# Optimization experiments

Measured on AMD Instinct MI355X. Metric: run time of the kernel, lower is better.

Reference implementation:

```python
import jax, jax.numpy as jnp
import numpy as np

B, I, H = 8192, 1024, 1024

def setup_inputs() -> dict:
    key = jax.random.key(0)
    ks = jax.random.split(key, 6)
    s_in = 1.0 / np.sqrt(I)
    s_h = 1.0 / np.sqrt(H)
    return {
        "x": jax.random.normal(ks[0], (B, I), jnp.float32),
        "h_prev": jax.random.normal(ks[1], (B, H), jnp.float32),
        "c_prev": jax.random.normal(ks[2], (B, H), jnp.float32),
        "Wx": jax.random.normal(ks[3], (4, H, I), jnp.float32) * s_in,   # gate order: input, forget, cell, output
        "Wh": jax.random.normal(ks[4], (4, H, H), jnp.float32) * s_h,
        "bh": jax.random.normal(ks[5], (4, H), jnp.float32) * s_h,
    }

def reference(x, h_prev, c_prev, Wx, Wh, bh):
    # Fused: 2 batched GEMMs for all 4 gates -> [B, 4, H]
    gates = (jnp.einsum('bi,ghi->bgh', x, Wx)
             + jnp.einsum('bk,ghk->bgh', h_prev, Wh)
             + bh[None, :, :])
    i = jax.nn.sigmoid(gates[:, 0])
    f = jax.nn.sigmoid(gates[:, 1])
    g = jnp.tanh(gates[:, 2])
    o = jax.nn.sigmoid(gates[:, 3])
    c_next = f * c_prev + i * g
    h_next = o * jnp.tanh(c_next)
    return (h_next, c_next)
```

## Files before the change

kernel.cpp:

```cpp
#include <hip/hip_runtime.h>
#include <hip/hip_bf16.h>
#include <stdint.h>

#define B_DIM 8192
#define I_DIM 1024
#define H_DIM 1024
#define KTOT  2048
#define NTILES 32

typedef __attribute__((ext_vector_type(8))) short short8;
typedef __attribute__((ext_vector_type(4))) float f32x4;

static __device__ __forceinline__ short f2b(float f) {
    __bf16 h = (__bf16)f;
    return __builtin_bit_cast(short, h);
}

static __device__ __forceinline__ short8 pack8(float4 a, float4 b) {
    short8 s;
    s[0] = f2b(a.x); s[1] = f2b(a.y); s[2] = f2b(a.z); s[3] = f2b(a.w);
    s[4] = f2b(b.x); s[5] = f2b(b.y); s[6] = f2b(b.z); s[7] = f2b(b.w);
    return s;
}

static __device__ __forceinline__ float sigmoid_f(float x) {
    return 1.0f / (1.0f + __expf(-x));
}

static __device__ __forceinline__ float tanh_fast(float x) {
    x = fminf(fmaxf(x, -15.0f), 15.0f);
    float e = __expf(2.0f * x);
    return (e - 1.0f) / (e + 1.0f);
}

static __device__ __forceinline__ void load_lds16(const void* gptr, void* lptr) {
    __builtin_amdgcn_global_load_lds(
        (const __attribute__((address_space(1))) uint32_t*)gptr,
        (__attribute__((address_space(3))) uint32_t*)lptr, 16, 0, 0);
}

#define GA_GROUPS (512 * 32 * 2 * 64)
#define GB_GROUPS (256 * 32 * 2 * 64)

__global__ __launch_bounds__(256) void convert_kernel(
    const float* __restrict__ x, const float* __restrict__ h,
    const float* __restrict__ wx, const float* __restrict__ wh,
    short* __restrict__ Aw, short* __restrict__ Bw)
{
    const int64_t total = (int64_t)GA_GROUPS + GB_GROUPS;
    for (int64_t g = (int64_t)blockIdx.x * blockDim.x + threadIdx.x; g < total;
         g += (int64_t)gridDim.x * blockDim.x) {
        const float* src;
        short* dst;
        if (g < GA_GROUPS) {
            const int lane = (int)(g & 63);
            const int rest = (int)(g >> 6);
            const int kh   = rest & 1;
            const int tk   = (rest >> 1) & 31;
            const int mfrag = rest >> 6;
            const int row = (mfrag << 4) + (lane & 15);
            const int k   = (tk << 6) + (kh << 5) + ((lane >> 4) << 3);
            src = (k < 1024) ? (x + (size_t)row * 1024 + k)
                             : (h + (size_t)row * 1024 + (k - 1024));
            dst = Aw + (size_t)g * 8;
        } else {
            const int64_t gb = g - GA_GROUPS;
            const int lane = (int)(gb & 63);
            const int rest = (int)(gb >> 6);
            const int kh   = rest & 1;
            const int tk   = (rest >> 1) & 31;
            const int nfrag = rest >> 6;
            const int cf   = nfrag & 15;
            const int bn   = nfrag >> 4;
            const int gate = cf & 3;
            const int col  = (bn << 6) + ((cf >> 2) << 4) + (lane & 15);
            const int k    = (tk << 6) + (kh << 5) + ((lane >> 4) << 3);
            src = (k < 1024) ? (wx + ((size_t)(gate << 10) + col) * 1024 + k)
                             : (wh + ((size_t)(gate << 10) + col) * 1024 + (k - 1024));
            dst = Bw + (size_t)gb * 8;
        }
        float4 v0 = ((const float4*)src)[0];
        float4 v1 = ((const float4*)src)[1];
        *(short8*)dst = pack8(v0, v1);
    }
}


#define AOFF(d, kp, f) ((d) * 16384 + (kp) * 8192 + (f) * 512)
#define BOFF(d, kp, f) (32768 + (d) * 16384 + (kp) * 8192 + (f) * 512)

#define STAGE_A(dn, kh, tkp) \
    load_lds16(aSrc0 + (tkp) * 1024 + (kh) * 512, &smem[AOFF(dn, kh, 2 * w)]); \
    load_lds16(aSrc1 + (tkp) * 1024 + (kh) * 512, &smem[AOFF(dn, kh, 2 * w + 1)]);

#define STAGE_B(dn, kh, tkp) \
    load_lds16(bSrc0 + (tkp) * 1024 + (kh) * 512, &smem[BOFF(dn, kh, 2 * w)]); \
    load_lds16(bSrc1 + (tkp) * 1024 + (kh) * 512, &smem[BOFF(dn, kh, 2 * w + 1)]);

#define VM4 asm volatile("s_waitcnt vmcnt(4)" ::: "memory");

#define PH(d, kp, mh, AV, BV, STAGE_STMT, EXTRAWAIT) do { \
    _Pragma("unroll") \
    for (int j = 0; j < 4; ++j) \
        BV[j] = *(const short8*)&smem[BOFF(d, kp, wn * 4 + j) + lane * 8]; \
    _Pragma("unroll") \
    for (int i = 0; i < 4; ++i) \
        AV[i] = *(const short8*)&smem[AOFF(d, kp, wm * 8 + (mh) * 4 + i) + lane * 8]; \
    STAGE_STMT \
    __builtin_amdgcn_s_barrier(); \
    __builtin_amdgcn_s_setprio(1); \
    _Pragma("unroll") \
    for (int i = 0; i < 4; ++i) \
        _Pragma("unroll") \
        for (int j = 0; j < 4; ++j) \
            acc[(mh) * 4 + i][j] = __builtin_amdgcn_mfma_f32_16x16x32_bf16( \
                AV[i], BV[j], acc[(mh) * 4 + i][j], 0, 0, 0); \
    __builtin_amdgcn_s_setprio(0); \
    EXTRAWAIT \
    __builtin_amdgcn_s_barrier(); \
} while (0)

#define TILE(d, tn) do { \
    PH(d, 0, 0, avA, bvA, STAGE_A(d ^ 1, 0, tn), ); \
    PH(d, 0, 1, avB, bvB, STAGE_B(d ^ 1, 0, tn), VM4); \
    PH(d, 1, 0, avA, bvA, STAGE_A(d ^ 1, 1, tn), ); \
    PH(d, 1, 1, avB, bvB, STAGE_B(d ^ 1, 1, tn), VM4); \
} while (0)

__global__ __launch_bounds__(512, 2) void lstm_gemm8_kernel(
    const short* __restrict__ Aw, const short* __restrict__ Bw,
    const float* __restrict__ cprev, const float* __restrict__ bh,
    float* __restrict__ out)
{
    extern __shared__ __align__(16) short smem[];

    int bid = blockIdx.x;
    bid = (bid & 7) * 64 + (bid >> 3);
    const int bm = bid >> 4;
    const int bn = bid & 15;
    const int m0 = bm * 256;
    const int h0 = bn * 64;

    const int t    = threadIdx.x;
    const int lane = t & 63;
    const int w    = t >> 6;
    const int wm   = w >> 2;
    const int wn   = w & 3;
    const int lc   = lane & 15;

    const short* aSrc0 = Aw + (size_t)(bm * 16 + 2 * w + 0) * 32768 + lane * 8;
    const short* aSrc1 = Aw + (size_t)(bm * 16 + 2 * w + 1) * 32768 + lane * 8;
    const short* bSrc0 = Bw + (size_t)(bn * 16 + 2 * w + 0) * 32768 + lane * 8;
    const short* bSrc1 = Bw + (size_t)(bn * 16 + 2 * w + 1) * 32768 + lane * 8;

    f32x4 acc[8][4] = {};
    short8 avA[4], avB[4], bvA[4], bvB[4];

    STAGE_A(0, 0, 0)
    STAGE_B(0, 0, 0)
    STAGE_A(0, 1, 0)
    STAGE_B(0, 1, 0)
    asm volatile("s_waitcnt vmcnt(0)" ::: "memory");
    __builtin_amdgcn_s_barrier();

    #pragma unroll 1
    for (int tk2 = 0; tk2 < 16; ++tk2) {
        const int t1  = 2 * tk2 + 1;
        const int tp1 = (t1 + 1 < NTILES) ? t1 + 1 : t1;
        TILE(0, t1);
        TILE(1, tp1);
    }
    asm volatile("s_waitcnt vmcnt(0)" ::: "memory");

    const int rg = lane >> 4;
    const int h  = h0 + wn * 16 + lc;
    const float b_i = bh[0 * H_DIM + h];
    const float b_f = bh[1 * H_DIM + h];
    const float b_g = bh[2 * H_DIM + h];
    const float b_o = bh[3 * H_DIM + h];

    #pragma unroll
    for (int mf = 0; mf < 8; ++mf) {
        #pragma unroll
        for (int r = 0; r < 4; ++r) {
            const int row = m0 + wm * 128 + mf * 16 + rg * 4 + r;
            const float pi = acc[mf][0][r] + b_i;
            const float pf = acc[mf][1][r] + b_f;
            const float pg = acc[mf][2][r] + b_g;
            const float po = acc[mf][3][r] + b_o;
            const float iv = sigmoid_f(pi);
            const float fv = sigmoid_f(pf);
            const float gv = tanh_fast(pg);
            const float ov = sigmoid_f(po);
            const float cp = cprev[(size_t)row * H_DIM + h];
            const float cn = fv * cp + iv * gv;
            const float hn = ov * tanh_fast(cn);
            out[(size_t)row * H_DIM + h] = hn;
            out[(size_t)B_DIM * H_DIM + (size_t)row * H_DIM + h] = cn;
        }
    }
}

static __device__ __forceinline__ int swz(int row, int k) {
    int byte = (row << 7) + (k << 1);
    byte ^= (row & 7) << 4;
    return byte >> 1;
}

__global__ __launch_bounds__(256, 2) void lstm_fallback_kernel(
    const float* __restrict__ x, const float* __restrict__ hprev,
    const float* __restrict__ cprev, const float* __restrict__ Wx,
    const float* __restrict__ Wh, const float* __restrict__ bh,
    float* __restrict__ out)
{
    __shared__ __align__(16) short As[128 * 64];
    __shared__ __align__(16) short Bs[128 * 64];

    int bid = blockIdx.x;
    bid = (bid & 7) * 256 + (bid >> 3);
    const int mt = bid >> 5;
    const int ht = bid & 31;
    const int m0 = mt * 128;
    const int h0 = ht * 32;

    const int t    = threadIdx.x;
    const int lane = t & 63;
    const int w    = t >> 6;
    const int wr   = w >> 1;
    const int wc   = w & 1;

    const int srow = t >> 3;
    const int sk   = (t & 7) * 8;

    f32x4 acc[4][4] = {};

    #pragma unroll 1
    for (int phase = 0; phase < 2; ++phase) {
        const float* __restrict__ Ap = phase ? hprev : x;
        const float* __restrict__ Bp = phase ? Wh : Wx;
        #pragma unroll 1
        for (int kk = 0; kk < 1024; kk += 64) {
            __syncthreads();
            #pragma unroll
            for (int p = 0; p < 4; ++p) {
                const int row = srow + p * 32;
                const float4* src = (const float4*)(Ap + (size_t)(m0 + row) * I_DIM + kk + sk);
                *(short8*)&As[swz(row, sk)] = pack8(src[0], src[1]);
            }
            #pragma unroll
            for (int p = 0; p < 4; ++p) {
                const int n    = srow + p * 32;
                const int gate = (n >> 4) & 3;
                const int hcol = h0 + ((n >> 6) << 4) + (n & 15);
                const float4* src = (const float4*)(Bp + (size_t)((gate << 10) + hcol) * 1024 + kk + sk);
                *(short8*)&Bs[swz(n, sk)] = pack8(src[0], src[1]);
            }
            __syncthreads();
            #pragma unroll
            for (int ks = 0; ks < 2; ++ks) {
                const int kb = ks * 32 + ((lane >> 4) << 3);
                short8 a[4], b[4];
                #pragma unroll
                for (int m = 0; m < 4; ++m)
                    a[m] = *(const short8*)&As[swz(wr * 64 + m * 16 + (lane & 15), kb)];
                #pragma unroll
                for (int j = 0; j < 4; ++j)
                    b[j] = *(const short8*)&Bs[swz(wc * 64 + j * 16 + (lane & 15), kb)];
                #pragma unroll
                for (int m = 0; m < 4; ++m)
                    #pragma unroll
                    for (int j = 0; j < 4; ++j)
                        acc[m][j] = __builtin_amdgcn_mfma_f32_16x16x32_bf16(a[m], b[j], acc[m][j], 0, 0, 0);
            }
        }
    }

    const int cl = lane & 15;
    const int rg = lane >> 4;
    const int h  = h0 + wc * 16 + cl;
    const float b_i = bh[0 * H_DIM + h];
    const float b_f = bh[1 * H_DIM + h];
    const float b_g = bh[2 * H_DIM + h];
    const float b_o = bh[3 * H_DIM + h];

    #pragma unroll
    for (int m = 0; m < 4; ++m) {
        #pragma unroll
        for (int r = 0; r < 4; ++r) {
            const int row = m0 + wr * 64 + m * 16 + rg * 4 + r;
            const float pi = acc[m][0][r] + b_i;
            const float pf = acc[m][1][r] + b_f;
            const float pg = acc[m][2][r] + b_g;
            const float po = acc[m][3][r] + b_o;
            const float iv = sigmoid_f(pi);
            const float fv = sigmoid_f(pf);
            const float gv = tanh_fast(pg);
            const float ov = sigmoid_f(po);
            const float cp = cprev[(size_t)row * H_DIM + h];
            const float cn = fv * cp + iv * gv;
            const float hn = ov * tanh_fast(cn);
            out[(size_t)row * H_DIM + h] = hn;
            out[(size_t)B_DIM * H_DIM + (size_t)row * H_DIM + h] = cn;
        }
    }
}

extern "C" void kernel_launch(void* const* d_in, const int* in_sizes, int n_in,
                              void* d_out, int out_size, void* d_ws, size_t ws_size,
                              hipStream_t stream) {
    const float* x     = (const float*)d_in[0];
    const float* hprev = (const float*)d_in[1];
    const float* cprev = (const float*)d_in[2];
    const float* Wx    = (const float*)d_in[3];
    const float* Wh    = (const float*)d_in[4];
    const float* bh    = (const float*)d_in[5];
    float* out = (float*)d_out;

    const size_t need = ((size_t)B_DIM * 2048 + (size_t)4096 * 2048) * sizeof(short);
    if (ws_size >= need && d_ws != nullptr) {
        (void)hipFuncSetAttribute((const void*)lstm_gemm8_kernel,
                                  hipFuncAttributeMaxDynamicSharedMemorySize, 131072);
        short* Aw = (short*)d_ws;
        short* Bw = Aw + (size_t)512 * 32768;
        hipLaunchKernelGGL(convert_kernel, dim3(4096), dim3(256), 0, stream,
                           x, hprev, Wx, Wh, Aw, Bw);
        hipLaunchKernelGGL(lstm_gemm8_kernel, dim3(512), dim3(512), 131072, stream,
                           Aw, Bw, cprev, bh, out);
    } else {
        hipLaunchKernelGGL(lstm_fallback_kernel, dim3(2048), dim3(256), 0, stream,
                           x, hprev, cprev, Wx, Wh, bh, out);
    }
}
```

Baseline: 154.2 us.

## Replace 256x64 ping-pong GEMM with smaller 128x64 tile for higher occupancy

The hand-scheduled 256-row tile kernel with 128KB dynamic LDS and multi-phase ping-pong staging is replaced by a 128-row tile kernel using 48KB static LDS, half the accumulators, and a simple double-buffered loop over 64 K-steps of 32. Launch bounds move to 4 blocks per CU and the grid doubles to 1024 blocks, with a new XCD-aware block mapping. The aim is to hide latency through thread-level parallelism instead of intra-wave scheduling. In exchange, each K-step ends with a full vmcnt(0) wait and barrier, and B-tile reuse per block is lower, so global and L2 traffic rises.

```diff
diff --git a/kernel.cpp b/kernel.cpp
--- a/kernel.cpp
+++ b/kernel.cpp
@@ -5,8 +5,6 @@
 #define B_DIM 8192
 #define I_DIM 1024
 #define H_DIM 1024
-#define KTOT  2048
-#define NTILES 32
 
 typedef __attribute__((ext_vector_type(8))) short short8;
 typedef __attribute__((ext_vector_type(4))) float f32x4;
@@ -85,61 +83,20 @@
     }
 }
 
-
-#define AOFF(d, kp, f) ((d) * 16384 + (kp) * 8192 + (f) * 512)
-#define BOFF(d, kp, f) (32768 + (d) * 16384 + (kp) * 8192 + (f) * 512)
-
-#define STAGE_A(dn, kh, tkp) \
-    load_lds16(aSrc0 + (tkp) * 1024 + (kh) * 512, &smem[AOFF(dn, kh, 2 * w)]); \
-    load_lds16(aSrc1 + (tkp) * 1024 + (kh) * 512, &smem[AOFF(dn, kh, 2 * w + 1)]);
-
-#define STAGE_B(dn, kh, tkp) \
-    load_lds16(bSrc0 + (tkp) * 1024 + (kh) * 512, &smem[BOFF(dn, kh, 2 * w)]); \
-    load_lds16(bSrc1 + (tkp) * 1024 + (kh) * 512, &smem[BOFF(dn, kh, 2 * w + 1)]);
-
-#define VM4 asm volatile("s_waitcnt vmcnt(4)" ::: "memory");
-
-#define PH(d, kp, mh, AV, BV, STAGE_STMT, EXTRAWAIT) do { \
-    _Pragma("unroll") \
-    for (int j = 0; j < 4; ++j) \
-        BV[j] = *(const short8*)&smem[BOFF(d, kp, wn * 4 + j) + lane * 8]; \
-    _Pragma("unroll") \
-    for (int i = 0; i < 4; ++i) \
-        AV[i] = *(const short8*)&smem[AOFF(d, kp, wm * 8 + (mh) * 4 + i) + lane * 8]; \
-    STAGE_STMT \
-    __builtin_amdgcn_s_barrier(); \
-    __builtin_amdgcn_s_setprio(1); \
-    _Pragma("unroll") \
-    for (int i = 0; i < 4; ++i) \
-        _Pragma("unroll") \
-        for (int j = 0; j < 4; ++j) \
-            acc[(mh) * 4 + i][j] = __builtin_amdgcn_mfma_f32_16x16x32_bf16( \
-                AV[i], BV[j], acc[(mh) * 4 + i][j], 0, 0, 0); \
-    __builtin_amdgcn_s_setprio(0); \
-    EXTRAWAIT \
-    __builtin_amdgcn_s_barrier(); \
-} while (0)
-
-#define TILE(d, tn) do { \
-    PH(d, 0, 0, avA, bvA, STAGE_A(d ^ 1, 0, tn), ); \
-    PH(d, 0, 1, avB, bvB, STAGE_B(d ^ 1, 0, tn), VM4); \
-    PH(d, 1, 0, avA, bvA, STAGE_A(d ^ 1, 1, tn), ); \
-    PH(d, 1, 1, avB, bvB, STAGE_B(d ^ 1, 1, tn), VM4); \
-} while (0)
-
-__global__ __launch_bounds__(512, 2) void lstm_gemm8_kernel(
+__global__ __launch_bounds__(512, 4) void lstm_gemm_tlp_kernel(
     const short* __restrict__ Aw, const short* __restrict__ Bw,
     const float* __restrict__ cprev, const float* __restrict__ bh,
     float* __restrict__ out)
 {
-    extern __shared__ __align__(16) short smem[];
-
-    int bid = blockIdx.x;
-    bid = (bid & 7) * 64 + (bid >> 3);
-    const int bm = bid >> 4;
-    const int bn = bid & 15;
-    const int m0 = bm * 256;
-    const int h0 = bn * 64;
+    __shared__ __align__(16) short smem[24576];
+
+    const int bid = blockIdx.x;
+    const int xcd = bid & 7;
+    const int c   = bid >> 3;
+    const int bm  = c >> 1;
+    const int bn  = 2 * xcd + (c & 1);
+    const int m0  = bm * 128;
+    const int h0  = bn * 64;
 
     const int t    = threadIdx.x;
     const int lane = t & 63;
@@ -148,29 +105,48 @@
     const int wn   = w & 3;
     const int lc   = lane & 15;
 
-    const short* aSrc0 = Aw + (size_t)(bm * 16 + 2 * w + 0) * 32768 + lane * 8;
-    const short* aSrc1 = Aw + (size_t)(bm * 16 + 2 * w + 1) * 32768 + lane * 8;
-    const short* bSrc0 = Bw + (size_t)(bn * 16 + 2 * w + 0) * 32768 + lane * 8;
+    const short* aSrc  = Aw + (size_t)(bm * 8  + w)         * 32768 + lane * 8;
+    const short* bSrc0 = Bw + (size_t)(bn * 16 + 2 * w)     * 32768 + lane * 8;
     const short* bSrc1 = Bw + (size_t)(bn * 16 + 2 * w + 1) * 32768 + lane * 8;
 
-    f32x4 acc[8][4] = {};
-    short8 avA[4], avB[4], bvA[4], bvB[4];
-
-    STAGE_A(0, 0, 0)
-    STAGE_B(0, 0, 0)
-    STAGE_A(0, 1, 0)
-    STAGE_B(0, 1, 0)
+    f32x4 acc[4][4] = {};
+
+    load_lds16(aSrc,  &smem[w * 512]);
+    load_lds16(bSrc0, &smem[4096 + (2 * w) * 512]);
+    load_lds16(bSrc1, &smem[4096 + (2 * w + 1) * 512]);
     asm volatile("s_waitcnt vmcnt(0)" ::: "memory");
     __builtin_amdgcn_s_barrier();
 
     #pragma unroll 1
-    for (int tk2 = 0; tk2 < 16; ++tk2) {
-        const int t1  = 2 * tk2 + 1;
-        const int tp1 = (t1 + 1 < NTILES) ? t1 + 1 : t1;
-        TILE(0, t1);
-        TILE(1, tp1);
-    }
-    asm volatile("s_waitcnt vmcnt(0)" ::: "memory");
+    for (int tk = 0; tk < 64; ++tk) {
+        const int d  = (tk & 1) * 12288;
+        const int dn = 12288 - d;
+        const int tp = (tk + 1 < 64) ? tk + 1 : tk;
+
+        short8 bv[4], av[4];
+        #pragma unroll
+        for (int j = 0; j < 4; ++j)
+            bv[j] = *(const short8*)&smem[d + 4096 + (wn * 4 + j) * 512 + lane * 8];
+        #pragma unroll
+        for (int i = 0; i < 4; ++i)
+            av[i] = *(const short8*)&smem[d + (wm * 4 + i) * 512 + lane * 8];
+
+        load_lds16(aSrc  + tp * 512, &smem[dn + w * 512]);
+        load_lds16(bSrc0 + tp * 512, &smem[dn + 4096 + (2 * w) * 512]);
+        load_lds16(bSrc1 + tp * 512, &smem[dn + 4096 + (2 * w + 1) * 512]);
+
+        __builtin_amdgcn_s_setprio(1);
+        #pragma unroll
+        for (int i = 0; i < 4; ++i)
+            #pragma unroll
+            for (int j = 0; j < 4; ++j)
+                acc[i][j] = __builtin_amdgcn_mfma_f32_16x16x32_bf16(
+                    av[i], bv[j], acc[i][j], 0, 0, 0);
+        __builtin_amdgcn_s_setprio(0);
+
+        asm volatile("s_waitcnt vmcnt(0)" ::: "memory");
+        __builtin_amdgcn_s_barrier();
+    }
 
     const int rg = lane >> 4;
     const int h  = h0 + wn * 16 + lc;
@@ -180,10 +156,10 @@
     const float b_o = bh[3 * H_DIM + h];
 
     #pragma unroll
-    for (int mf = 0; mf < 8; ++mf) {
+    for (int mf = 0; mf < 4; ++mf) {
         #pragma unroll
         for (int r = 0; r < 4; ++r) {
-            const int row = m0 + wm * 128 + mf * 16 + rg * 4 + r;
+            const int row = m0 + wm * 64 + mf * 16 + rg * 4 + r;
             const float pi = acc[mf][0][r] + b_i;
             const float pf = acc[mf][1][r] + b_f;
             const float pg = acc[mf][2][r] + b_g;
@@ -318,13 +294,11 @@
 
     const size_t need = ((size_t)B_DIM * 2048 + (size_t)4096 * 2048) * sizeof(short);
     if (ws_size >= need && d_ws != nullptr) {
-        (void)hipFuncSetAttribute((const void*)lstm_gemm8_kernel,
-                                  hipFuncAttributeMaxDynamicSharedMemorySize, 131072);
         short* Aw = (short*)d_ws;
         short* Bw = Aw + (size_t)512 * 32768;
         hipLaunchKernelGGL(convert_kernel, dim3(4096), dim3(256), 0, stream,
                            x, hprev, Wx, Wh, Aw, Bw);
-        hipLaunchKernelGGL(lstm_gemm8_kernel, dim3(512), dim3(512), 131072, stream,
+        hipLaunchKernelGGL(lstm_gemm_tlp_kernel, dim3(1024), dim3(512), 0, stream,
                            Aw, Bw, cprev, bh, out);
     } else {
         hipLaunchKernelGGL(lstm_fallback_kernel, dim3(2048), dim3(256), 0, stream,
```

Measured after the change: 149.1 us. 3.4% less time.

## Replace double-buffered K tiles with a four-slot ring prefetching three steps ahead

Applied to the files above, without the earlier changes.

The GEMM main loop moves from a two-buffer scheme (64-wide K tiles split into halves) to a four-slot ring of 32-wide K steps in LDS. Loads are issued three steps ahead, with a vmcnt(8) wait. Each step reuses the B fragments across both M halves, so B is read from LDS once per step instead of once per M half. The aim is deeper latency hiding for global-to-LDS loads. In exchange there are more barriers per K element, since there are twice as many steps, each with three barriers.

```diff
diff --git a/kernel.cpp b/kernel.cpp
--- a/kernel.cpp
+++ b/kernel.cpp
@@ -5,8 +5,6 @@
 #define B_DIM 8192
 #define I_DIM 1024
 #define H_DIM 1024
-#define KTOT  2048
-#define NTILES 32
 
 typedef __attribute__((ext_vector_type(8))) short short8;
 typedef __attribute__((ext_vector_type(4))) float f32x4;
@@ -85,49 +83,10 @@
     }
 }
 
-
-#define AOFF(d, kp, f) ((d) * 16384 + (kp) * 8192 + (f) * 512)
-#define BOFF(d, kp, f) (32768 + (d) * 16384 + (kp) * 8192 + (f) * 512)
-
-#define STAGE_A(dn, kh, tkp) \
-    load_lds16(aSrc0 + (tkp) * 1024 + (kh) * 512, &smem[AOFF(dn, kh, 2 * w)]); \
-    load_lds16(aSrc1 + (tkp) * 1024 + (kh) * 512, &smem[AOFF(dn, kh, 2 * w + 1)]);
-
-#define STAGE_B(dn, kh, tkp) \
-    load_lds16(bSrc0 + (tkp) * 1024 + (kh) * 512, &smem[BOFF(dn, kh, 2 * w)]); \
-    load_lds16(bSrc1 + (tkp) * 1024 + (kh) * 512, &smem[BOFF(dn, kh, 2 * w + 1)]);
-
-#define VM4 asm volatile("s_waitcnt vmcnt(4)" ::: "memory");
-
-#define PH(d, kp, mh, AV, BV, STAGE_STMT, EXTRAWAIT) do { \
-    _Pragma("unroll") \
-    for (int j = 0; j < 4; ++j) \
-        BV[j] = *(const short8*)&smem[BOFF(d, kp, wn * 4 + j) + lane * 8]; \
-    _Pragma("unroll") \
-    for (int i = 0; i < 4; ++i) \
-        AV[i] = *(const short8*)&smem[AOFF(d, kp, wm * 8 + (mh) * 4 + i) + lane * 8]; \
-    STAGE_STMT \
-    __builtin_amdgcn_s_barrier(); \
-    __builtin_amdgcn_s_setprio(1); \
-    _Pragma("unroll") \
-    for (int i = 0; i < 4; ++i) \
-        _Pragma("unroll") \
-        for (int j = 0; j < 4; ++j) \
-            acc[(mh) * 4 + i][j] = __builtin_amdgcn_mfma_f32_16x16x32_bf16( \
-                AV[i], BV[j], acc[(mh) * 4 + i][j], 0, 0, 0); \
-    __builtin_amdgcn_s_setprio(0); \
-    EXTRAWAIT \
-    __builtin_amdgcn_s_barrier(); \
-} while (0)
-
-#define TILE(d, tn) do { \
-    PH(d, 0, 0, avA, bvA, STAGE_A(d ^ 1, 0, tn), ); \
-    PH(d, 0, 1, avB, bvB, STAGE_B(d ^ 1, 0, tn), VM4); \
-    PH(d, 1, 0, avA, bvA, STAGE_A(d ^ 1, 1, tn), ); \
-    PH(d, 1, 1, avB, bvB, STAGE_B(d ^ 1, 1, tn), VM4); \
-} while (0)
-
-__global__ __launch_bounds__(512, 2) void lstm_gemm8_kernel(
+#define AOFF(r, f) ((r) * 16384 + (f) * 512)
+#define BOFF(r, f) ((r) * 16384 + 8192 + (f) * 512)
+
+__global__ __launch_bounds__(512, 2) void lstm_gemm_p8_kernel(
     const short* __restrict__ Aw, const short* __restrict__ Bw,
     const float* __restrict__ cprev, const float* __restrict__ bh,
     float* __restrict__ out)
@@ -148,28 +107,78 @@
     const int wn   = w & 3;
     const int lc   = lane & 15;
 
-    const short* aSrc0 = Aw + (size_t)(bm * 16 + 2 * w + 0) * 32768 + lane * 8;
+    const short* aSrc0 = Aw + (size_t)(bm * 16 + 2 * w)     * 32768 + lane * 8;
     const short* aSrc1 = Aw + (size_t)(bm * 16 + 2 * w + 1) * 32768 + lane * 8;
-    const short* bSrc0 = Bw + (size_t)(bn * 16 + 2 * w + 0) * 32768 + lane * 8;
+    const short* bSrc0 = Bw + (size_t)(bn * 16 + 2 * w)     * 32768 + lane * 8;
     const short* bSrc1 = Bw + (size_t)(bn * 16 + 2 * w + 1) * 32768 + lane * 8;
 
     f32x4 acc[8][4] = {};
-    short8 avA[4], avB[4], bvA[4], bvB[4];
-
-    STAGE_A(0, 0, 0)
-    STAGE_B(0, 0, 0)
-    STAGE_A(0, 1, 0)
-    STAGE_B(0, 1, 0)
-    asm volatile("s_waitcnt vmcnt(0)" ::: "memory");
+
+#define SA(r, p) \
+    load_lds16(aSrc0 + (p) * 512, &smem[AOFF(r, 2 * w)]); \
+    load_lds16(aSrc1 + (p) * 512, &smem[AOFF(r, 2 * w + 1)]);
+#define SB(r, p) \
+    load_lds16(bSrc0 + (p) * 512, &smem[BOFF(r, 2 * w)]); \
+    load_lds16(bSrc1 + (p) * 512, &smem[BOFF(r, 2 * w + 1)]);
+
+#define STEP(r, pr, p) do { \
+    short8 bv[4], av[4]; \
+    _Pragma("unroll") \
+    for (int j = 0; j < 4; ++j) \
+        bv[j] = *(const short8*)&smem[BOFF(r, wn * 4 + j) + lane * 8]; \
+    _Pragma("unroll") \
+    for (int i = 0; i < 4; ++i) \
+        av[i] = *(const short8*)&smem[AOFF(r, wm * 8 + i) + lane * 8]; \
+    SA(pr, p) \
+    __builtin_amdgcn_s_barrier(); \
+    __builtin_amdgcn_s_setprio(1); \
+    _Pragma("unroll") \
+    for (int i = 0; i < 4; ++i) \
+        _Pragma("unroll") \
+        for (int j = 0; j < 4; ++j) \
+            acc[i][j] = __builtin_amdgcn_mfma_f32_16x16x32_bf16( \
+                av[i], bv[j], acc[i][j], 0, 0, 0); \
+    __builtin_amdgcn_s_setprio(0); \
+    __builtin_amdgcn_s_barrier(); \
+    short8 aw[4]; \
+    _Pragma("unroll") \
+    for (int i = 0; i < 4; ++i) \
+        aw[i] = *(const short8*)&smem[AOFF(r, wm * 8 + 4 + i) + lane * 8]; \
+    SB(pr, p) \
+    __builtin_amdgcn_s_barrier(); \
+    __builtin_amdgcn_s_setprio(1); \
+    _Pragma("unroll") \
+    for (int i = 0; i < 4; ++i) \
+        _Pragma("unroll") \
+        for (int j = 0; j < 4; ++j) \
+            acc[4 + i][j] = __builtin_amdgcn_mfma_f32_16x16x32_bf16( \
+                aw[i], bv[j], acc[4 + i][j], 0, 0, 0); \
+    __builtin_amdgcn_s_setprio(0); \
+    asm volatile("s_waitcnt vmcnt(8)" ::: "memory"); \
+    __builtin_amdgcn_s_barrier(); \
+} while (0)
+
+    SA(0, 0) SB(0, 0)
+    SA(1, 1) SB(1, 1)
+    SA(2, 2) SB(2, 2)
+    asm volatile("s_waitcnt vmcnt(8)" ::: "memory");
     __builtin_amdgcn_s_barrier();
 
     #pragma unroll 1
-    for (int tk2 = 0; tk2 < 16; ++tk2) {
-        const int t1  = 2 * tk2 + 1;
-        const int tp1 = (t1 + 1 < NTILES) ? t1 + 1 : t1;
-        TILE(0, t1);
-        TILE(1, tp1);
-    }
+    for (int s4 = 0; s4 < 16; ++s4) {
+        const int b4 = 4 * s4;
+        const int p0 = (b4 + 3 < 64) ? b4 + 3 : 63;
+        const int p1 = (b4 + 4 < 64) ? b4 + 4 : 63;
+        const int p2 = (b4 + 5 < 64) ? b4 + 5 : 63;
+        const int p3 = (b4 + 6 < 64) ? b4 + 6 : 63;
+        STEP(0, 3, p0);
+        STEP(1, 0, p1);
+        STEP(2, 1, p2);
+        STEP(3, 2, p3);
+    }
+#undef STEP
+#undef SA
+#undef SB
     asm volatile("s_waitcnt vmcnt(0)" ::: "memory");
 
     const int rg = lane >> 4;
@@ -318,13 +327,13 @@
 
     const size_t need = ((size_t)B_DIM * 2048 + (size_t)4096 * 2048) * sizeof(short);
     if (ws_size >= need && d_ws != nullptr) {
-        (void)hipFuncSetAttribute((const void*)lstm_gemm8_kernel,
+        (void)hipFuncSetAttribute((const void*)lstm_gemm_p8_kernel,
                                   hipFuncAttributeMaxDynamicSharedMemorySize, 131072);
         short* Aw = (short*)d_ws;
         short* Bw = Aw + (size_t)512 * 32768;
         hipLaunchKernelGGL(convert_kernel, dim3(4096), dim3(256), 0, stream,
                            x, hprev, Wx, Wh, Aw, Bw);
-        hipLaunchKernelGGL(lstm_gemm8_kernel, dim3(512), dim3(512), 131072, stream,
+        hipLaunchKernelGGL(lstm_gemm_p8_kernel, dim3(512), dim3(512), 131072, stream,
                            Aw, Bw, cprev, bh, out);
     } else {
         hipLaunchKernelGGL(lstm_fallback_kernel, dim3(2048), dim3(256), 0, stream,
```

After: 149.9 us. 1.03x faster.
